# Kernel tuning notes

Measured on AMD Instinct MI355X. Metric: run time of the kernel, lower is better.

The kernel has to match this reference:

```python
import jax, jax.numpy as jnp
import numpy as np

B, S, D = 4, 2048, 1024
H, A = 16, 64


def setup_inputs() -> dict:
    key = jax.random.key(0)
    ks = jax.random.split(key, 9)
    return {
        "q": jax.random.normal(ks[0], (B, S, D), dtype=jnp.float32),
        "k": jax.random.normal(ks[1], (B, S, D), dtype=jnp.float32),
        "v": jax.random.normal(ks[2], (B, S, D), dtype=jnp.float32),
        "Wq": jax.random.normal(ks[3], (H, D, A), dtype=jnp.float32) * (1.0 / np.sqrt(D)),
        "bq": jax.random.normal(ks[4], (H, A), dtype=jnp.float32) * 0.01,
        "Wk": jax.random.normal(ks[5], (H, D, A), dtype=jnp.float32) * (1.0 / np.sqrt(D)),
        "bk": jax.random.normal(ks[6], (H, A), dtype=jnp.float32) * 0.01,
        "Wv": jax.random.normal(ks[7], (H, D, A), dtype=jnp.float32) * (1.0 / np.sqrt(D)),
        "bv": jax.random.normal(ks[8], (H, A), dtype=jnp.float32) * 0.01,
    }


def reference(q, k, v, Wq, bq, Wk, bk, Wv, bv):
    # Per-head linear projections (batched over heads): [B,H,S,A]
    qh = jnp.einsum("bsd,hda->bhsa", q, Wq) + bq[None, :, None, :]
    kh = jnp.einsum("bsd,hda->bhsa", k, Wk) + bk[None, :, None, :]
    vh = jnp.einsum("bsd,hda->bhsa", v, Wv) + bv[None, :, None, :]
    # NOTE: original has NO 1/sqrt(d) scaling and no mask.
    scores = jnp.einsum("bhqa,bhka->bhqk", qh, kh)  # [B,H,S,S]
    weights = jax.nn.softmax(scores, axis=-1)
    attn = jnp.einsum("bhqk,bhka->bhqa", weights, vh)  # [B,H,S,A]
    # concat heads on last dim: [B,S,H*A]
    return jnp.transpose(attn, (0, 2, 1, 3)).reshape(q.shape[0], q.shape[1], -1)
```

## Files before the change

kernel.cpp:

```cpp
#include <hip/hip_runtime.h>
#include <stdint.h>

#define B_ 4
#define S_ 2048
#define D_ 1024
#define H_ 16
#define A_ 64
#define M_ (B_*S_)
#define BH_ (B_*H_)
#define INV_LN2 1.4426950408889634f

typedef _Float16 f16x8 __attribute__((ext_vector_type(8)));
typedef float    f32x4 __attribute__((ext_vector_type(4)));

__device__ __forceinline__ uint32_t f2h(float f) {
    _Float16 h = (_Float16)f;
    return (uint32_t)__builtin_bit_cast(uint16_t, h);
}

__device__ __forceinline__ float exp2f_fast(float x) {
    return __builtin_amdgcn_exp2f(x);
}

__device__ __forceinline__ uint32_t pkrtz(float a, float b) {
    return __builtin_bit_cast(uint32_t, __builtin_amdgcn_cvt_pkrtz(a, b));
}

__device__ __forceinline__ int swz(int row, int col) {
    return (row * 64 + col) ^ ((row & 7) << 3);
}

__global__ __launch_bounds__(256) void prep_w(
    const float* __restrict__ Wq, const float* __restrict__ Wk, const float* __restrict__ Wv,
    uint16_t* __restrict__ Wt)
{
    __shared__ float tile[64][65];
    const int dt = blockIdx.x, h = blockIdx.y, p = blockIdx.z;
    const float* W = (p == 0) ? Wq : (p == 1) ? Wk : Wv;
    const float sc = (p == 0) ? INV_LN2 : 1.0f;
    const float* src = W + (h * D_ + dt * 64) * A_;
    const int t = threadIdx.x;
    const int r0 = t >> 4, c4 = (t & 15) * 4;
    #pragma unroll
    for (int i = 0; i < 4; i++) {
        int r = r0 + i * 16;
        float4 x = *(const float4*)(src + r * A_ + c4);
        tile[r][c4] = x.x; tile[r][c4 + 1] = x.y; tile[r][c4 + 2] = x.z; tile[r][c4 + 3] = x.w;
    }
    __syncthreads();
    uint16_t* dst = Wt + (p * H_ + h) * (A_ * D_) + dt * 64;
    #pragma unroll
    for (int i = 0; i < 4; i++) {
        int a = r0 + i * 16;
        int d4 = (t & 15) * 4;
        uint2 o2;
        o2.x = f2h(tile[d4][a] * sc)     | (f2h(tile[d4 + 1][a] * sc) << 16);
        o2.y = f2h(tile[d4 + 2][a] * sc) | (f2h(tile[d4 + 3][a] * sc) << 16);
        *(uint2*)(dst + a * D_ + d4) = o2;
    }
}

__global__ __launch_bounds__(512) void proj_kernel(
    const float* __restrict__ qsrc, const float* __restrict__ ksrc, const float* __restrict__ vsrc,
    const uint16_t* __restrict__ Wt,
    const float* __restrict__ bq, const float* __restrict__ bk, const float* __restrict__ bv,
    uint16_t* __restrict__ qh, uint16_t* __restrict__ kh, uint16_t* __restrict__ vpv)
{
    __shared__ __align__(16) float    Asf[2][128 * 32];
    __shared__ __align__(16) uint16_t Bs[2][256 * 32];
    const int p = blockIdx.z, nt = blockIdx.y, mt = blockIdx.x;
    const int t = threadIdx.x, lane = t & 63, w = t >> 6;
    const int wr = w >> 2, wc = w & 3;
    const int lr = lane & 15, lg = lane >> 4;
    const int Mbase = mt * 128;
    const float* Af = (p == 0) ? qsrc : (p == 1) ? ksrc : vsrc;

    const int ar = t >> 3;
    const int asl = (t & 7) ^ (ar & 7);
    const float* asrc = Af + (size_t)(Mbase + ar) * D_ + asl * 4;

    const int br = t >> 2;
    const int bsl = (t & 3) ^ ((br >> 1) & 3);
    const uint16_t* bsrc[2];
    #pragma unroll
    for (int i = 0; i < 2; i++) {
        int row = br + 128 * i;
        bsrc[i] = Wt + ((size_t)(p * H_ + nt * 4 + (row >> 6)) * A_ + (row & 63)) * D_ + bsl * 8;
    }

    f32x4 acc[4][4] = {};

    #define PSTAGE(buf, kkv) do {                                                                  \
        __builtin_amdgcn_global_load_lds(asrc + (kkv),                                             \
                                         (char*)(&Asf[buf][0]) + w * 1024,        16, 0, 0);       \
        __builtin_amdgcn_global_load_lds(asrc + (kkv) + (size_t)64 * D_,                           \
                                         (char*)(&Asf[buf][0]) + 8192 + w * 1024, 16, 0, 0);       \
        __builtin_amdgcn_global_load_lds(bsrc[0] + (kkv),                                          \
                                         (char*)(&Bs[buf][0]) + w * 1024,         16, 0, 0);       \
        __builtin_amdgcn_global_load_lds(bsrc[1] + (kkv),                                          \
                                         (char*)(&Bs[buf][0]) + 8192 + w * 1024,  16, 0, 0);       \
    } while (0)

    const int NKS = D_ / 32;
    PSTAGE(0, 0);

    for (int ks = 0; ks < NKS; ks++) {
        const int cur = ks & 1;
        if (ks + 1 < NKS) {
            PSTAGE(cur ^ 1, (ks + 1) * 32);
            asm volatile("s_waitcnt vmcnt(4)" ::: "memory");
        } else {
            asm volatile("s_waitcnt vmcnt(0)" ::: "memory");
        }
        __builtin_amdgcn_s_barrier();
        __builtin_amdgcn_sched_barrier(0);

        f16x8 af[4], bf[4];
        #pragma unroll
        for (int mb = 0; mb < 4; mb++) {
            const int r = wr * 64 + mb * 16 + lr;
            const int c = r & 7;
            const float* base = &Asf[cur][0] + r * 32;
            f32x4 lo = *(const f32x4*)(base + (((2 * lg)     ^ c) << 2));
            f32x4 hi = *(const f32x4*)(base + (((2 * lg + 1) ^ c) << 2));
            uint4 u;
            u.x = pkrtz(lo[0], lo[1]); u.y = pkrtz(lo[2], lo[3]);
            u.z = pkrtz(hi[0], hi[1]); u.w = pkrtz(hi[2], hi[3]);
            af[mb] = __builtin_bit_cast(f16x8, u);
        }
        #pragma unroll
        for (int nb = 0; nb < 4; nb++) {
            const int r = wc * 64 + nb * 16 + lr;
            const int ph = lg ^ ((r >> 1) & 3);
            bf[nb] = *(const f16x8*)(&Bs[cur][0] + r * 32 + ph * 8);
        }
        #pragma unroll
        for (int mb = 0; mb < 4; mb++) {
            #pragma unroll
            for (int nb = 0; nb < 4; nb++)
                acc[mb][nb] = __builtin_amdgcn_mfma_f32_16x16x32_f16(af[mb], bf[nb], acc[mb][nb], 0, 0, 0);
        }
        __builtin_amdgcn_s_barrier();
        __builtin_amdgcn_sched_barrier(0);
    }
    #undef PSTAGE

    const int h = nt * 4 + wc;
    const int b = Mbase >> 11;
    const int bh = b * H_ + h;
    const int sbase = Mbase & (S_ - 1);
    const float* bias = ((p == 0) ? bq : (p == 1) ? bk : bv) + h * A_;
    const float bsc = (p == 0) ? INV_LN2 : 1.0f;
    #pragma unroll
    for (int mb = 0; mb < 4; mb++) {
        #pragma unroll
        for (int nb = 0; nb < 4; nb++) {
            const int a = nb * 16 + lr;
            const float bia = bias[a] * bsc;
            const int s0 = sbase + wr * 64 + mb * 16 + 4 * lg;
            if (p < 2) {
                uint16_t* o = (p == 0) ? qh : kh;
                #pragma unroll
                for (int r = 0; r < 4; r++)
                    o[(bh * S_ + s0 + r) * A_ + a] = (uint16_t)f2h(acc[mb][nb][r] + bia);
            } else {
                const int kt2 = s0 >> 6, kv0 = s0 & 63;
                const int kb2 = kv0 >> 5, jhi = (kv0 >> 4) & 1, lg2 = (kv0 >> 2) & 3;
                uint2 pk2;
                pk2.x = f2h(acc[mb][nb][0] + bia) | (f2h(acc[mb][nb][1] + bia) << 16);
                pk2.y = f2h(acc[mb][nb][2] + bia) | (f2h(acc[mb][nb][3] + bia) << 16);
                *(uint2*)(vpv + ((size_t)((bh * 32 + kt2) * 512 + kb2 * 256 + lg2 * 64 + a)) * 8 + 4 * jhi) = pk2;
            }
        }
    }
}

__global__ __launch_bounds__(512, 8) void flash_kernel(
    const uint16_t* __restrict__ qh, const uint16_t* __restrict__ kh,
    const uint16_t* __restrict__ vpv, float* __restrict__ out)
{
    __shared__ __align__(16) uint16_t smem[24576];
    const int t = threadIdx.x, lane = t & 63, w = t >> 6;
    const int lr = lane & 15, lg = lane >> 4;

    const int flat = blockIdx.y * gridDim.x + blockIdx.x;
    const int nf = (flat & 7) * 128 + (flat >> 3);
    const int qt = nf & 15, bh = nf >> 4;
    const int b = bh >> 4, h = bh & (H_ - 1);

    f16x8 qf[2];
    {
        const uint16_t* qp = qh + (size_t)(bh * S_ + qt * 128 + w * 16 + lr) * A_ + 8 * lg;
        qf[0] = *(const f16x8*)(qp);
        qf[1] = *(const f16x8*)(qp + 32);
    }
    f16x8 ones;
    #pragma unroll
    for (int j = 0; j < 8; j++) ones[j] = (_Float16)1.0f;

    const int row0 = t >> 3;
    const int col0 = (t * 8) & 63;
    const int scol = col0 ^ ((row0 & 7) << 3);
    const uint16_t* kg = kh + (size_t)(bh * S_ + row0) * A_ + scol;
    const uint16_t* vg = vpv + (size_t)bh * (S_ * A_) + t * 8;

    f32x4 negm = {};
    f32x4 oacc[4] = {};
    f32x4 lsum = {};

    #define FSTAGE(buf, kt_) do {                                                         \
        __builtin_amdgcn_global_load_lds(kg + (size_t)(kt_) * (64 * A_),                  \
                                         smem + (buf) * 4096 + w * 512, 16, 0, 0);        \
        __builtin_amdgcn_global_load_lds(vg + (size_t)(kt_) * 4096,                       \
                                         smem + 12288 + (buf) * 4096 + w * 512, 16, 0, 0);\
    } while (0)

    const int NT = S_ / 64;
    FSTAGE(0, 0);
    FSTAGE(1, 1);

    int cur = 0;
    for (int kt = 0; kt < NT; kt++) {
        if (kt < NT - 1) asm volatile("s_waitcnt vmcnt(2)" ::: "memory");
        else             asm volatile("s_waitcnt vmcnt(0)" ::: "memory");
        __builtin_amdgcn_s_barrier();
        __builtin_amdgcn_sched_barrier(0);
        if (kt + 2 < NT) {
            int nb2 = cur + 2; if (nb2 >= 3) nb2 -= 3;
            FSTAGE(nb2, kt + 2);
        }
        __builtin_amdgcn_sched_barrier(0);
        const uint16_t* Kc = smem + cur * 4096;
        const uint16_t* Vc = smem + 12288 + cur * 4096;

        f32x4 sacc[4];
        __builtin_amdgcn_s_setprio(1);
        #pragma unroll
        for (int nb = 0; nb < 4; nb++) {
            f16x8 kf = *(const f16x8*)(Kc + swz(nb * 16 + lr, 8 * lg));
            sacc[nb] = __builtin_amdgcn_mfma_f32_16x16x32_f16(kf, qf[0], negm, 0, 0, 0);
        }
        #pragma unroll
        for (int nb = 0; nb < 4; nb++) {
            f16x8 kf = *(const f16x8*)(Kc + swz(nb * 16 + lr, 32 + 8 * lg));
            sacc[nb] = __builtin_amdgcn_mfma_f32_16x16x32_f16(kf, qf[1], sacc[nb], 0, 0, 0);
        }
        __builtin_amdgcn_s_setprio(0);

        float a0 = fmaxf(fmaxf(sacc[0][0], sacc[0][1]), sacc[0][2]);
        float a1 = fmaxf(fmaxf(sacc[0][3], sacc[1][0]), sacc[1][1]);
        float a2 = fmaxf(fmaxf(sacc[1][2], sacc[1][3]), sacc[2][0]);
        float a3 = fmaxf(fmaxf(sacc[2][1], sacc[2][2]), sacc[2][3]);
        float a4 = fmaxf(fmaxf(sacc[3][0], sacc[3][1]), sacc[3][2]);
        float pm = fmaxf(fmaxf(fmaxf(a0, a1), fmaxf(a2, a3)), fmaxf(a4, sacc[3][3]));

        if (__any(pm > 11.0f)) {
            float tm = fmaxf(pm, __shfl_xor(pm, 16));
            tm = fmaxf(tm, __shfl_xor(tm, 32));
            float delta = fmaxf(tm, 0.0f);
            float sc = exp2f_fast(-delta);
            #pragma unroll
            for (int r = 0; r < 4; r++) negm[r] -= delta;
            #pragma unroll
            for (int nb = 0; nb < 4; nb++) {
                #pragma unroll
                for (int r = 0; r < 4; r++) sacc[nb][r] -= delta;
            }
            float scr[4];
            #pragma unroll
            for (int r = 0; r < 4; r++) scr[r] = __shfl(sc, 4 * lg + r);
            #pragma unroll
            for (int r = 0; r < 4; r++) lsum[r] *= scr[r];
            #pragma unroll
            for (int nb = 0; nb < 4; nb++) {
                #pragma unroll
                for (int r = 0; r < 4; r++) oacc[nb][r] *= scr[r];
            }
        }

        f16x8 paf[2];
        #pragma unroll
        for (int kb2 = 0; kb2 < 2; kb2++) {
            float e[8];
            #pragma unroll
            for (int jh = 0; jh < 2; jh++) {
                #pragma unroll
                for (int r = 0; r < 4; r++)
                    e[jh * 4 + r] = exp2f_fast(sacc[2 * kb2 + jh][r]);
            }
            uint4 u;
            u.x = pkrtz(e[0], e[1]); u.y = pkrtz(e[2], e[3]);
            u.z = pkrtz(e[4], e[5]); u.w = pkrtz(e[6], e[7]);
            paf[kb2] = __builtin_bit_cast(f16x8, u);
        }

        __builtin_amdgcn_s_setprio(1);
        lsum = __builtin_amdgcn_mfma_f32_16x16x32_f16(paf[0], ones, lsum, 0, 0, 0);
        lsum = __builtin_amdgcn_mfma_f32_16x16x32_f16(paf[1], ones, lsum, 0, 0, 0);
        #pragma unroll
        for (int kb2 = 0; kb2 < 2; kb2++) {
            #pragma unroll
            for (int nb = 0; nb < 4; nb++) {
                f16x8 vf = *(const f16x8*)(Vc + ((kb2 * 4 + lg) * 64 + nb * 16 + lr) * 8);
                oacc[nb] = __builtin_amdgcn_mfma_f32_16x16x32_f16(paf[kb2], vf, oacc[nb], 0, 0, 0);
            }
        }
        __builtin_amdgcn_s_setprio(0);

        cur = (cur == 2) ? 0 : cur + 1;
    }
    #undef FSTAGE

    __syncthreads();
    float* outs = (float*)smem;
    #pragma unroll
    for (int r = 0; r < 4; r++) {
        const float inv = 1.0f / lsum[r];
        const int sl = w * 16 + 4 * lg + r;
        #pragma unroll
        for (int nb = 0; nb < 4; nb++)
            outs[sl * 64 + nb * 16 + lr] = oacc[nb][r] * inv;
    }
    __syncthreads();
    const int orow = t >> 4, oslot = t & 15;
    float* obase = out + (size_t)(b * S_ + qt * 128 + orow) * (H_ * A_) + h * A_ + oslot * 4;
    #pragma unroll
    for (int i = 0; i < 4; i++)
        *(float4*)(obase + (size_t)(32 * i) * (H_ * A_)) =
            *(const float4*)(outs + (orow + 32 * i) * 64 + oslot * 4);
}

extern "C" void kernel_launch(void* const* d_in, const int* in_sizes, int n_in,
                              void* d_out, int out_size, void* d_ws, size_t ws_size,
                              hipStream_t stream)
{
    const float* q  = (const float*)d_in[0];
    const float* k  = (const float*)d_in[1];
    const float* v  = (const float*)d_in[2];
    const float* Wq = (const float*)d_in[3];
    const float* bq = (const float*)d_in[4];
    const float* Wk = (const float*)d_in[5];
    const float* bk = (const float*)d_in[6];
    const float* Wv = (const float*)d_in[7];
    const float* bv = (const float*)d_in[8];
    float* out = (float*)d_out;

    uint8_t* ws = (uint8_t*)d_ws;
    const size_t SZ_H  = (size_t)BH_ * S_ * A_ * 2;
    uint16_t* qh  = (uint16_t*)(ws);
    uint16_t* kh  = (uint16_t*)(ws + SZ_H);
    uint16_t* vpv = (uint16_t*)(ws + 2 * SZ_H);
    uint16_t* Wt  = (uint16_t*)(ws + 3 * SZ_H);

    prep_w<<<dim3(16, H_, 3), 256, 0, stream>>>(Wq, Wk, Wv, Wt);
    proj_kernel<<<dim3(M_ / 128, 4, 3), 512, 0, stream>>>(q, k, v, Wt,
                                                          bq, bk, bv, qh, kh, vpv);
    flash_kernel<<<dim3(S_ / 128, BH_), 512, 0, stream>>>(qh, kh, vpv, out);
}
```

Before: 170.6 us.

## Convert projection A operand to fp16 once per stage via register staging

The projection kernel no longer streams fp32 activations straight into LDS with async loads. Each thread now loads its fp32 activation slice into registers, converts it to fp16 once, and writes a swizzled fp16 tile to LDS after the MFMA work. This removes the redundant per-wave fp32-to-fp16 conversion on LDS reads and halves the A-tile LDS footprint. The cost is register pressure, synchronous global loads that must finish before the LDS write and barrier, and a restructured barrier schedule; a launch-bounds occupancy hint is also added.

```diff
diff --git a/kernel.cpp b/kernel.cpp
--- a/kernel.cpp
+++ b/kernel.cpp
@@ -60,13 +60,13 @@
     }
 }
 
-__global__ __launch_bounds__(512) void proj_kernel(
+__global__ __launch_bounds__(512, 6) void proj_kernel(
     const float* __restrict__ qsrc, const float* __restrict__ ksrc, const float* __restrict__ vsrc,
     const uint16_t* __restrict__ Wt,
     const float* __restrict__ bq, const float* __restrict__ bk, const float* __restrict__ bv,
     uint16_t* __restrict__ qh, uint16_t* __restrict__ kh, uint16_t* __restrict__ vpv)
 {
-    __shared__ __align__(16) float    Asf[2][128 * 32];
+    __shared__ __align__(16) uint16_t As[2][128 * 32];
     __shared__ __align__(16) uint16_t Bs[2][256 * 32];
     const int p = blockIdx.z, nt = blockIdx.y, mt = blockIdx.x;
     const int t = threadIdx.x, lane = t & 63, w = t >> 6;
@@ -75,64 +75,64 @@
     const int Mbase = mt * 128;
     const float* Af = (p == 0) ? qsrc : (p == 1) ? ksrc : vsrc;
 
-    const int ar = t >> 3;
-    const int asl = (t & 7) ^ (ar & 7);
-    const float* asrc = Af + (size_t)(Mbase + ar) * D_ + asl * 4;
-
-    const int br = t >> 2;
-    const int bsl = (t & 3) ^ ((br >> 1) & 3);
+    const int ar  = t >> 2;
+    const int als = t & 3;
+    const int afx = (ar >> 1) & 3;
+    const float* asrc = Af + (size_t)(Mbase + ar) * D_ + als * 8;
+    const int awoff = ar * 32 + ((als ^ afx) * 8);
+
+    const int bslot = (t & 3) ^ (((t >> 2) >> 1) & 3);
     const uint16_t* bsrc[2];
     #pragma unroll
     for (int i = 0; i < 2; i++) {
-        int row = br + 128 * i;
-        bsrc[i] = Wt + ((size_t)(p * H_ + nt * 4 + (row >> 6)) * A_ + (row & 63)) * D_ + bsl * 8;
+        int row = (t >> 2) + 128 * i;
+        bsrc[i] = Wt + ((size_t)(p * H_ + nt * 4 + (row >> 6)) * A_ + (row & 63)) * D_ + bslot * 8;
     }
 
     f32x4 acc[4][4] = {};
 
-    #define PSTAGE(buf, kkv) do {                                                                  \
-        __builtin_amdgcn_global_load_lds(asrc + (kkv),                                             \
-                                         (char*)(&Asf[buf][0]) + w * 1024,        16, 0, 0);       \
-        __builtin_amdgcn_global_load_lds(asrc + (kkv) + (size_t)64 * D_,                           \
-                                         (char*)(&Asf[buf][0]) + 8192 + w * 1024, 16, 0, 0);       \
-        __builtin_amdgcn_global_load_lds(bsrc[0] + (kkv),                                          \
-                                         (char*)(&Bs[buf][0]) + w * 1024,         16, 0, 0);       \
-        __builtin_amdgcn_global_load_lds(bsrc[1] + (kkv),                                          \
-                                         (char*)(&Bs[buf][0]) + 8192 + w * 1024,  16, 0, 0);       \
+    #define BSTAGE(buf, kkv) do {                                                                  \
+        __builtin_amdgcn_global_load_lds(bsrc[0] + (kkv), (char*)(&Bs[buf][0]) + w * 1024,        16, 0, 0); \
+        __builtin_amdgcn_global_load_lds(bsrc[1] + (kkv), (char*)(&Bs[buf][0]) + 8192 + w * 1024, 16, 0, 0); \
     } while (0)
 
+    #define AWRITE(buf, v0, v1) do {                                                               \
+        uint4 u_;                                                                                  \
+        u_.x = pkrtz((v0).x, (v0).y); u_.y = pkrtz((v0).z, (v0).w);                                \
+        u_.z = pkrtz((v1).x, (v1).y); u_.w = pkrtz((v1).z, (v1).w);                                \
+        *(uint4*)(&As[buf][awoff]) = u_;                                                           \
+    } while (0)
+
+    {
+        BSTAGE(0, 0);
+        float4 a0 = *(const float4*)(asrc);
+        float4 a1 = *(const float4*)(asrc + 4);
+        asm volatile("s_waitcnt vmcnt(0)" ::: "memory");
+        AWRITE(0, a0, a1);
+        __syncthreads();
+    }
+
     const int NKS = D_ / 32;
-    PSTAGE(0, 0);
-
     for (int ks = 0; ks < NKS; ks++) {
-        const int cur = ks & 1;
-        if (ks + 1 < NKS) {
-            PSTAGE(cur ^ 1, (ks + 1) * 32);
-            asm volatile("s_waitcnt vmcnt(4)" ::: "memory");
-        } else {
-            asm volatile("s_waitcnt vmcnt(0)" ::: "memory");
-        }
-        __builtin_amdgcn_s_barrier();
-        __builtin_amdgcn_sched_barrier(0);
+        const int cur = ks & 1, nxt = cur ^ 1;
+        const bool hasNext = (ks + 1 < NKS);
+        float4 a0, a1;
+        if (hasNext) {
+            BSTAGE(nxt, (ks + 1) * 32);
+            a0 = *(const float4*)(asrc + (ks + 1) * 32);
+            a1 = *(const float4*)(asrc + (ks + 1) * 32 + 4);
+        }
 
         f16x8 af[4], bf[4];
         #pragma unroll
         for (int mb = 0; mb < 4; mb++) {
             const int r = wr * 64 + mb * 16 + lr;
-            const int c = r & 7;
-            const float* base = &Asf[cur][0] + r * 32;
-            f32x4 lo = *(const f32x4*)(base + (((2 * lg)     ^ c) << 2));
-            f32x4 hi = *(const f32x4*)(base + (((2 * lg + 1) ^ c) << 2));
-            uint4 u;
-            u.x = pkrtz(lo[0], lo[1]); u.y = pkrtz(lo[2], lo[3]);
-            u.z = pkrtz(hi[0], hi[1]); u.w = pkrtz(hi[2], hi[3]);
-            af[mb] = __builtin_bit_cast(f16x8, u);
+            af[mb] = *(const f16x8*)(&As[cur][r * 32 + ((lg ^ ((r >> 1) & 3)) * 8)]);
         }
         #pragma unroll
         for (int nb = 0; nb < 4; nb++) {
             const int r = wc * 64 + nb * 16 + lr;
-            const int ph = lg ^ ((r >> 1) & 3);
-            bf[nb] = *(const f16x8*)(&Bs[cur][0] + r * 32 + ph * 8);
+            bf[nb] = *(const f16x8*)(&Bs[cur][r * 32 + ((lg ^ ((r >> 1) & 3)) * 8)]);
         }
         #pragma unroll
         for (int mb = 0; mb < 4; mb++) {
@@ -140,10 +140,16 @@
             for (int nb = 0; nb < 4; nb++)
                 acc[mb][nb] = __builtin_amdgcn_mfma_f32_16x16x32_f16(af[mb], bf[nb], acc[mb][nb], 0, 0, 0);
         }
-        __builtin_amdgcn_s_barrier();
-        __builtin_amdgcn_sched_barrier(0);
-    }
-    #undef PSTAGE
+
+        if (hasNext) {
+            asm volatile("s_waitcnt vmcnt(0)" ::: "memory");
+            __builtin_amdgcn_sched_barrier(0);
+            AWRITE(nxt, a0, a1);
+            __syncthreads();
+        }
+    }
+    #undef BSTAGE
+    #undef AWRITE
 
     const int h = nt * 4 + wc;
     const int b = Mbase >> 11;
```

Measured after the change: 385.0 us. +125.6%, slower.
